# Kernel tuning notes

Measured on AMD Instinct MI355X. Metric: run time of the kernel, lower is better.

## Reference

```python
import jax, jax.numpy as jnp
import numpy as np

EMBED_DIM = 1024
NUM_HEADS = 16
HEAD_DIM = EMBED_DIM // NUM_HEADS
KERNEL = 3
PAD = KERNEL // 2
B, L = 4, 1024


def conv1d(x, w, b):
    # x: [B, D, L], w: [D_out, D_in, K], b: [D_out]; 'same' padding like nn.Conv1d(padding=K//2)
    y = jax.lax.conv_general_dilated(
        x, w, window_strides=(1,), padding=[(PAD, PAD)],
        dimension_numbers=('NCH', 'OIH', 'NCH'))
    return y + b[None, :, None]


def setup_inputs() -> dict:
    key = jax.random.key(0)
    ks = jax.random.split(key, 12)
    fan = EMBED_DIM * KERNEL
    bound = 1.0 / np.sqrt(fan)
    def wconv(k):
        return jax.random.uniform(k, (EMBED_DIM, EMBED_DIM, KERNEL), jnp.float32, -bound, bound)
    def bconv(k):
        return jax.random.uniform(k, (EMBED_DIM,), jnp.float32, -bound, bound)
    return {
        'query': jax.random.normal(ks[0], (B, L, EMBED_DIM), jnp.float32),
        'key': jax.random.normal(ks[1], (B, L, EMBED_DIM), jnp.float32),
        'value': jax.random.normal(ks[2], (B, L, EMBED_DIM), jnp.float32),
        'key_padding_mask': jax.random.randint(ks[3], (B, L), 0, 2) > 0,
        'attn_mask': jnp.zeros((L, L), jnp.float32),
        'q_w': wconv(ks[4]), 'q_b': bconv(ks[5]),
        'k_w': wconv(ks[6]), 'k_b': bconv(ks[7]),
        'v_w': wconv(ks[8]), 'v_b': bconv(ks[9]),
        'o_w': wconv(ks[10]), 'o_b': bconv(ks[11]),
    }


def reference(query, key, value, key_padding_mask, attn_mask,
              q_w, q_b, k_w, k_b, v_w, v_b, o_w, o_b):
    scale = HEAD_DIM ** -0.5
    # projections: [B, D, L]
    q = conv1d(jnp.swapaxes(query, 1, 2), q_w, q_b)
    k = conv1d(jnp.swapaxes(key, 1, 2), k_w, k_b)
    v = conv1d(jnp.swapaxes(value, 1, 2), v_w, v_b)
    # [B, H, d, L]
    q = q.reshape(B, NUM_HEADS, HEAD_DIM, L)
    k = k.reshape(B, NUM_HEADS, HEAD_DIM, L)
    v = v.reshape(B, NUM_HEADS, HEAD_DIM, L)
    # scores: [B, H, L, L]
    scores = jnp.einsum('bhdi,bhdj->bhij', q, k) * scale
    scores = scores + attn_mask[None, None, :, :]
    scores = jnp.where(key_padding_mask[:, None, None, :], -jnp.inf, scores)
    attn = jax.nn.softmax(scores, axis=-1)  # dropout p=0 (eval) -> identity
    out = jnp.einsum('bhij,bhdj->bhdi', attn, v)  # [B, H, d, L]
    out = out.reshape(B, EMBED_DIM, L)
    out = conv1d(out, o_w, o_b)
    return jnp.swapaxes(out, 1, 2)  # [B, L, D]
```

## Files before the change

### kernel.cpp

```cpp
#include <hip/hip_runtime.h>
#include <math.h>

#define NB 4
#define NL 1024
#define ND 1024
#define NH 16
#define HD 64

typedef __attribute__((ext_vector_type(8))) short bf16x8;
typedef __attribute__((ext_vector_type(4))) float f32x4;

static __device__ __forceinline__ unsigned short f32_to_bf16(float f) {
  unsigned u = __float_as_uint(f);
  u += 0x7FFFu + ((u >> 16) & 1u);
  return (unsigned short)(u >> 16);
}
static __device__ __forceinline__ float bf16_to_f32(unsigned short s) {
  return __uint_as_float(((unsigned)s) << 16);
}
static __device__ __forceinline__ float exp2_f(float x) {
  float r;
  asm("v_exp_f32 %0, %1" : "=v"(r) : "v"(x));
  return r;
}

static __device__ __forceinline__ void split8(float4 a, float4 b, bf16x8* hi, bf16x8* lo) {
  unsigned u[8] = {__float_as_uint(a.x), __float_as_uint(a.y),
                   __float_as_uint(a.z), __float_as_uint(a.w),
                   __float_as_uint(b.x), __float_as_uint(b.y),
                   __float_as_uint(b.z), __float_as_uint(b.w)};
  union { unsigned p[4]; bf16x8 v; } H, L;
#pragma unroll
  for (int p = 0; p < 4; ++p) {
    unsigned u0 = u[2 * p], u1 = u[2 * p + 1];
    H.p[p] = __builtin_amdgcn_perm(u1, u0, 0x07060302u);
    unsigned l0 = __float_as_uint(__uint_as_float(u0) - __uint_as_float(u0 & 0xFFFF0000u));
    unsigned l1 = __float_as_uint(__uint_as_float(u1) - __uint_as_float(u1 & 0xFFFF0000u));
    L.p[p] = __builtin_amdgcn_perm(l1, l0, 0x07060302u);
  }
  *hi = H.v; *lo = L.v;
}

__global__ __launch_bounds__(256) void wcvt_kernel(
    const float* __restrict__ w0, const float* __restrict__ w1,
    const float* __restrict__ w2, const float* __restrict__ w3,
    unsigned short* __restrict__ wb, int* __restrict__ flag)
{
  if (blockIdx.x == 0 && blockIdx.y == 0 && threadIdx.x == 0) flag[0] = 0;
  const int t = blockIdx.y;
  const int o = blockIdx.x;
  const float* w = (t == 0) ? w0 : (t == 1) ? w1 : (t == 2) ? w2 : w3;
  unsigned short* hi = wb + (size_t)t * 6 * (1u << 20);
  unsigned short* lo = hi + 3 * (1u << 20);
  const int tid = threadIdx.x;
  float v[12];
  const float* src = w + (size_t)o * (ND * 3) + tid * 12;
#pragma unroll
  for (int j = 0; j < 3; ++j) {
    float4 f = *(const float4*)(src + j * 4);
    v[j * 4 + 0] = f.x; v[j * 4 + 1] = f.y; v[j * 4 + 2] = f.z; v[j * 4 + 3] = f.w;
  }
#pragma unroll
  for (int k = 0; k < 3; ++k) {
    unsigned short hh[4], ll[4];
#pragma unroll
    for (int ii = 0; ii < 4; ++ii) {
      float x = v[ii * 3 + k];
      unsigned short h = f32_to_bf16(x);
      float r = x - bf16_to_f32(h);
      hh[ii] = h; ll[ii] = f32_to_bf16(r);
    }
    size_t dst = (size_t)k * (ND * ND) + (size_t)o * ND + tid * 4;
    *(ushort4*)&hi[dst] = make_ushort4(hh[0], hh[1], hh[2], hh[3]);
    *(ushort4*)&lo[dst] = make_ushort4(ll[0], ll[1], ll[2], ll[3]);
  }
}

__global__ __launch_bounds__(256) void amask_scan(
    const float* __restrict__ a, int* __restrict__ flag)
{
  size_t i = ((size_t)blockIdx.x * 256 + threadIdx.x) * 4;
  float4 v = *(const float4*)&a[i];
  if (v.x != 0.f || v.y != 0.f || v.z != 0.f || v.w != 0.f) atomicOr(flag, 1);
}

__global__ __launch_bounds__(256, 3) void conv_mfma2(
    const float* X0, const float* X1, const float* X2,
    const unsigned short* __restrict__ wb,
    const float* b0, const float* b1, const float* b2,
    float* Y0, float* Y1, float* Y2, int mode)
{
  __shared__ float Af[128 * 32];
  __shared__ unsigned short Bh[128 * 32];
  __shared__ unsigned short Bl[128 * 32];

  const int tid = threadIdx.x, lane = tid & 63, wave = tid >> 6;
  const int lin = blockIdx.x + 8 * (blockIdx.y + 32 * blockIdx.z);
  const int g = lin & 7, t = lin >> 3;
  const int nb = (g & 3) * 2 + (t & 1);
  const int mb = (g >> 2) * 16 + ((t >> 1) & 15);
  const int z  = t >> 5;
  const int n0 = nb * 128, m0 = mb * 128;
  const int b = m0 >> 10, l0v = m0 & (NL - 1);

  const float* X = (mode == 0) ? (z == 0 ? X0 : (z == 1 ? X1 : X2)) : X0;
  const unsigned short* Wh = (mode == 0) ? wb + (size_t)z * 6 * (1u << 20) : wb;
  const unsigned short* Wl = Wh + 3 * (1u << 20);

  const int wm = (wave >> 1) * 64, wn = (wave & 1) * 64;
  const int mrow = lane & 15, quad = lane >> 4;
  const int r16 = lane >> 2, cs = lane & 3;
  const int src_chunk = (cs - (r16 >> 1)) & 3;
  const int bswz = ((quad + (mrow >> 1)) & 3) * 8;

  f32x4 acc[4][4] = {};

  const int kbeg = (mode == 0) ? 0 : z;
  const int kend = (mode == 0) ? 3 : z + 1;
  for (int koff = kbeg; koff < kend; ++koff) {
    const bool edge_lo = (l0v == 0 && koff == 0);
    const bool edge_hi = (l0v == NL - 128 && koff == 2);
    for (int i0 = 0; i0 < ND; i0 += 32) {
#pragma unroll
      for (int s = 0; s < 2; ++s) {
        const int seg = wave * 2 + s;
        const size_t goff = ((size_t)koff << 20) +
                            (size_t)(n0 + seg * 16 + r16) * ND + i0 + src_chunk * 8;
        __builtin_amdgcn_global_load_lds(
            (const __attribute__((address_space(1))) unsigned int*)(Wh + goff),
            (__attribute__((address_space(3))) unsigned int*)&Bh[seg * 512], 16, 0, 0);
        __builtin_amdgcn_global_load_lds(
            (const __attribute__((address_space(1))) unsigned int*)(Wl + goff),
            (__attribute__((address_space(3))) unsigned int*)&Bl[seg * 512], 16, 0, 0);
      }
#pragma unroll
      for (int j = 0; j < 4; ++j) {
        const int s = (wave * 4 + j) * 64 + lane;
        const int row = s >> 3, sir = s & 7;
        const int chunk = (sir - (row & 7)) & 7;
        int l = l0v + row + koff - 1;
        l = (l < 0) ? 0 : (l > NL - 1 ? NL - 1 : l);
        const float* gp = X + ((size_t)(b << 10) + l) * ND + i0 + chunk * 4;
        __builtin_amdgcn_global_load_lds(
            (const __attribute__((address_space(1))) unsigned int*)gp,
            (__attribute__((address_space(3))) unsigned int*)&Af[(wave * 4 + j) * 256],
            16, 0, 0);
      }
      __syncthreads();
      if (edge_lo || edge_hi) {
        const int er = edge_lo ? 0 : 127;
        if (tid < 8) *(float4*)&Af[er * 32 + tid * 4] = make_float4(0.f, 0.f, 0.f, 0.f);
        __syncthreads();
      }
      bf16x8 ah[4], al[4];
#pragma unroll
      for (int mi = 0; mi < 4; ++mi) {
        const int row = wm + mi * 16 + mrow, r7 = row & 7;
        float4 fa = *(const float4*)&Af[row * 32 + (((quad * 2) + r7) & 7) * 4];
        float4 fb = *(const float4*)&Af[row * 32 + (((quad * 2 + 1) + r7) & 7) * 4];
        split8(fa, fb, &ah[mi], &al[mi]);
      }
#pragma unroll
      for (int ni = 0; ni < 4; ++ni) {
        const int brow = wn + ni * 16 + mrow;
        bf16x8 bh = *(const bf16x8*)&Bh[brow * 32 + bswz];
        bf16x8 bl = *(const bf16x8*)&Bl[brow * 32 + bswz];
#pragma unroll
        for (int mi = 0; mi < 4; ++mi) {
          acc[mi][ni] = __builtin_amdgcn_mfma_f32_16x16x32_bf16(ah[mi], bh, acc[mi][ni], 0, 0, 0);
          acc[mi][ni] = __builtin_amdgcn_mfma_f32_16x16x32_bf16(ah[mi], bl, acc[mi][ni], 0, 0, 0);
          acc[mi][ni] = __builtin_amdgcn_mfma_f32_16x16x32_bf16(al[mi], bh, acc[mi][ni], 0, 0, 0);
        }
      }
      __syncthreads();
    }
  }

  if (mode == 0) {
    const float* bias = (z == 0) ? b0 : (z == 1 ? b1 : b2);
    unsigned short* U = (unsigned short*)Y0;
    const size_t PLs = (size_t)NB * NL * ND / NH * NH;
    if (z < 2) {
      unsigned short* Ph = U + (size_t)(2 * z) * PLs;
      unsigned short* Pl = Ph + PLs;
      const float sc = (z == 0) ? 0.18033688011112042f : 1.0f;
#pragma unroll
      for (int ni = 0; ni < 4; ++ni) {
        const int n = n0 + wn + ni * 16 + mrow;
        const float bv = bias[n];
        const int h = n >> 6, dd = n & 63;
        const int bh = b * NH + h;
#pragma unroll
        for (int mi = 0; mi < 4; ++mi) {
          const int mbase = m0 + wm + mi * 16 + quad * 4;
          f32x4 v = acc[mi][ni];
#pragma unroll
          for (int r = 0; r < 4; ++r) {
            const int l = (mbase + r) & (NL - 1);
            const float val = (v[r] + bv) * sc;
            const unsigned u = __float_as_uint(val);
            const unsigned short hh = (unsigned short)(u >> 16);
            const float res = val - __uint_as_float(u & 0xFFFF0000u);
            const unsigned short ll = (unsigned short)(__float_as_uint(res) >> 16);
            const size_t off = ((size_t)bh * NL + l) * HD + dd;
            Ph[off] = hh; Pl[off] = ll;
          }
        }
      }
    } else {
      unsigned short* Pv = U + (size_t)4 * PLs;
#pragma unroll
      for (int ni = 0; ni < 4; ++ni) {
        const int n = n0 + wn + ni * 16 + mrow;
        const float bv = bias[n];
        const int h = n >> 6, dd = n & 63;
        const int bh = b * NH + h;
#pragma unroll
        for (int mi = 0; mi < 4; ++mi) {
          const int mbase = m0 + wm + mi * 16 + quad * 4;
          const int lb = mbase & (NL - 1);
          f32x4 v = acc[mi][ni];
          ushort4 s4 = make_ushort4(f32_to_bf16(v[0] + bv), f32_to_bf16(v[1] + bv),
                                    f32_to_bf16(v[2] + bv), f32_to_bf16(v[3] + bv));
          *(ushort4*)&Pv[((size_t)bh * HD + dd) * NL + lb] = s4;
        }
      }
    }
  } else {
    float* P = Y0 + (size_t)z * ((size_t)NB * NL * ND);
#pragma unroll
    for (int ni = 0; ni < 4; ++ni) {
      const int n = n0 + wn + ni * 16 + mrow;
#pragma unroll
      for (int mi = 0; mi < 4; ++mi) {
        const int mbase = m0 + wm + mi * 16 + quad * 4;
        f32x4 v = acc[mi][ni];
#pragma unroll
        for (int r = 0; r < 4; ++r) {
          const int l = (mbase + r) & (NL - 1);
          P[((size_t)(b << 10) + l) * ND + n] = v[r];
        }
      }
    }
  }
}

__global__ __launch_bounds__(256) void reduce_kernel(
    const float* __restrict__ P, const float* __restrict__ bias, float* __restrict__ out)
{
  const size_t S = (size_t)NB * NL * ND;
  const size_t idx = ((size_t)blockIdx.x * 256 + threadIdx.x) * 4;
  const int n = (int)(idx & (ND - 1));
  float4 p0 = *(const float4*)&P[idx];
  float4 p1 = *(const float4*)&P[idx + S];
  float4 p2 = *(const float4*)&P[idx + 2 * S];
  float4 bv = *(const float4*)&bias[n];
  float4 r;
  r.x = p0.x + p1.x + p2.x + bv.x;
  r.y = p0.y + p1.y + p2.y + bv.y;
  r.z = p0.z + p1.z + p2.z + bv.z;
  r.w = p0.w + p1.w + p2.w + bv.w;
  *(float4*)&out[idx] = r;
}

__global__ __launch_bounds__(256, 3) void attn_mfma(
    const unsigned short* __restrict__ U, const int* __restrict__ kpm,
    const float* __restrict__ amask, const int* __restrict__ aflagp,
    float* __restrict__ AO)
{
  __shared__ __align__(16) unsigned short S[3 * 4096];
  __shared__ __align__(16) float Fm[NL];
  unsigned short* Kh = S;
  unsigned short* Kl = S + 4096;
  unsigned short* Vt = S + 8192;

  const int tid = threadIdx.x, lane = tid & 63, wave = tid >> 6;
  const int c = lane & 15, quad = lane >> 4;
  const int lin = blockIdx.x;
  const int bh = (lin & 7) + 8 * (lin >> 7);
  const int mt = (lin >> 3) & 15;
  const int b = bh >> 4;
  const int m0 = mt * 64;
  const int aflag = *aflagp;
  const int mrow = wave * 16 + c;
  const int gm = m0 + mrow;

  const size_t PLs = (size_t)4096 * 1024;
  const unsigned short* qTh = U;
  const unsigned short* qTl = U + PLs;
  const unsigned short* kTh = U + 2 * PLs;
  const unsigned short* kTl = U + 3 * PLs;
  const unsigned short* vTt = U + 4 * PLs;

  const int srow = lane >> 3;
  const int slot = lane & 7;
  const int chunk = (slot - srow) & 7;

#pragma unroll
  for (int q = 0; q < 4; ++q) {
    const int pl = q >> 1;
    const int i = wave * 2 + (q & 1);
    const int row = i * 8 + srow;
    const unsigned short* src = (pl ? qTl : qTh) +
        ((size_t)bh * NL + m0 + row) * HD + chunk * 8;
    unsigned short* dst = (pl ? Kl : Kh) + i * 512;
    __builtin_amdgcn_global_load_lds(
        (const __attribute__((address_space(1))) unsigned int*)src,
        (__attribute__((address_space(3))) unsigned int*)dst, 16, 0, 0);
  }
  {
    int4 kv = *(const int4*)&kpm[b * NL + tid * 4];
    float4 f;
    f.x = kv.x ? -INFINITY : 0.f;
    f.y = kv.y ? -INFINITY : 0.f;
    f.z = kv.z ? -INFINITY : 0.f;
    f.w = kv.w ? -INFINITY : 0.f;
    *(float4*)&Fm[tid * 4] = f;
  }
  __syncthreads();
  bf16x8 qbh[2], qbl[2];
#pragma unroll
  for (int kb = 0; kb < 2; ++kb) {
    const int cso = ((kb * 4 + quad + mrow) & 7) * 8;
    qbh[kb] = *(const bf16x8*)&Kh[mrow * 64 + cso];
    qbl[kb] = *(const bf16x8*)&Kl[mrow * 64 + cso];
  }

  f32x4 acc[4] = {};
  float m_r = -INFINITY, l_r = 0.0f;

  for (int n0t = 0; n0t < NL; n0t += 64) {
    __syncthreads();

#pragma unroll
    for (int q = 0; q < 6; ++q) {
      const int pl = q >> 1;
      const int i = wave * 2 + (q & 1);
      const int row = i * 8 + srow;
      const unsigned short* src;
      unsigned short* dst;
      if (pl == 0)      { src = kTh + ((size_t)bh * NL + n0t + row) * HD + chunk * 8; dst = Kh + i * 512; }
      else if (pl == 1) { src = kTl + ((size_t)bh * NL + n0t + row) * HD + chunk * 8; dst = Kl + i * 512; }
      else              { src = vTt + ((size_t)bh * HD + row) * NL + n0t + chunk * 8; dst = Vt + i * 512; }
      __builtin_amdgcn_global_load_lds(
          (const __attribute__((address_space(1))) unsigned int*)src,
          (__attribute__((address_space(3))) unsigned int*)dst, 16, 0, 0);
    }

    float mval[4][4];
#pragma unroll
    for (int nf = 0; nf < 4; ++nf) {
      float4 fm = *(const float4*)&Fm[n0t + nf * 16 + quad * 4];
      mval[nf][0] = fm.x; mval[nf][1] = fm.y; mval[nf][2] = fm.z; mval[nf][3] = fm.w;
    }
    if (aflag) {
#pragma unroll
      for (int nf = 0; nf < 4; ++nf)
#pragma unroll
        for (int r = 0; r < 4; ++r) {
          const int gn = n0t + nf * 16 + quad * 4 + r;
          mval[nf][r] += amask[(size_t)gm * NL + gn] * 1.4426950408889634f;
        }
    }
    __syncthreads();

    f32x4 sa[4] = {};
    __builtin_amdgcn_s_setprio(1);
#pragma unroll
    for (int kb = 0; kb < 2; ++kb)
#pragma unroll
      for (int nf = 0; nf < 4; ++nf) {
        const int row = nf * 16 + c;
        const int cso = ((kb * 4 + quad + row) & 7) * 8;
        bf16x8 kah = *(const bf16x8*)&Kh[row * 64 + cso];
        bf16x8 kal = *(const bf16x8*)&Kl[row * 64 + cso];
        sa[nf] = __builtin_amdgcn_mfma_f32_16x16x32_bf16(kah, qbh[kb], sa[nf], 0, 0, 0);
        sa[nf] = __builtin_amdgcn_mfma_f32_16x16x32_bf16(kah, qbl[kb], sa[nf], 0, 0, 0);
        sa[nf] = __builtin_amdgcn_mfma_f32_16x16x32_bf16(kal, qbh[kb], sa[nf], 0, 0, 0);
      }
    __builtin_amdgcn_s_setprio(0);

    float p[4][4];
    float tmax = -INFINITY;
#pragma unroll
    for (int nf = 0; nf < 4; ++nf)
#pragma unroll
      for (int r = 0; r < 4; ++r) {
        float s = sa[nf][r] + mval[nf][r];
        p[nf][r] = s;
        tmax = fmaxf(tmax, s);
      }
    tmax = fmaxf(tmax, __shfl_xor(tmax, 16));
    tmax = fmaxf(tmax, __shfl_xor(tmax, 32));
    float rs = 0.f;
    if (__all(tmax - m_r <= 8.0f)) {
      const float msafe = m_r;
#pragma unroll
      for (int nf = 0; nf < 4; ++nf)
#pragma unroll
        for (int r = 0; r < 4; ++r) {
          float e = exp2_f(p[nf][r] - msafe);
          p[nf][r] = e;
          rs += e;
        }
      rs += __shfl_xor(rs, 16);
      rs += __shfl_xor(rs, 32);
      l_r += rs;
    } else {
      const float newm = fmaxf(m_r, tmax);
      const float msafe = (newm == -INFINITY) ? 0.f : newm;
      const float alpha = exp2_f(m_r - msafe);
#pragma unroll
      for (int nf = 0; nf < 4; ++nf)
#pragma unroll
        for (int r = 0; r < 4; ++r) {
          float e = exp2_f(p[nf][r] - msafe);
          p[nf][r] = e;
          rs += e;
        }
      rs += __shfl_xor(rs, 16);
      rs += __shfl_xor(rs, 32);
      l_r = l_r * alpha + rs;
      m_r = newm;
#pragma unroll
      for (int df = 0; df < 4; ++df) {
        acc[df][0] *= alpha; acc[df][1] *= alpha;
        acc[df][2] *= alpha; acc[df][3] *= alpha;
      }
    }

    unsigned q16[4][2];
#pragma unroll
    for (int nf = 0; nf < 4; ++nf)
#pragma unroll
      for (int w = 0; w < 2; ++w)
        q16[nf][w] = (unsigned)f32_to_bf16(p[nf][2 * w]) |
                     ((unsigned)f32_to_bf16(p[nf][2 * w + 1]) << 16);

#pragma unroll
    for (int kb = 0; kb < 2; ++kb) {
      union { unsigned d[4]; bf16x8 v; } pb;
#pragma unroll
      for (int w = 0; w < 4; ++w) {
        const int addr = ((((quad & 1) * 2 + (w >> 1)) * 16 + c) << 2);
        unsigned v0 = __builtin_amdgcn_ds_bpermute(addr, (int)q16[2 * kb][w & 1]);
        unsigned v1 = __builtin_amdgcn_ds_bpermute(addr, (int)q16[2 * kb + 1][w & 1]);
        pb.d[w] = (quad >> 1) ? v1 : v0;
      }
      __builtin_amdgcn_s_setprio(1);
#pragma unroll
      for (int df = 0; df < 4; ++df) {
        const int row = df * 16 + c;
        const int cso = ((kb * 4 + quad + row) & 7) * 8;
        bf16x8 va = *(const bf16x8*)&Vt[row * 64 + cso];
        acc[df] = __builtin_amdgcn_mfma_f32_16x16x32_bf16(va, pb.v, acc[df], 0, 0, 0);
      }
      __builtin_amdgcn_s_setprio(0);
    }
  }

  __syncthreads();
  const float inv = 1.0f / l_r;
  float* Ob = (float*)S + wave * (16 * 68);
#pragma unroll
  for (int df = 0; df < 4; ++df)
#pragma unroll
    for (int r = 0; r < 4; ++r)
      Ob[c * 68 + df * 16 + quad * 4 + r] = acc[df][r] * inv;
  __syncthreads();
  const int mr2 = lane >> 2, cq2 = lane & 3;
  const int h = bh & 15;
#pragma unroll
  for (int ii = 0; ii < 4; ++ii) {
    const int chunk2 = cq2 * 4 + ii;
    float4 v = *(const float4*)&Ob[mr2 * 68 + chunk2 * 4];
    *(float4*)&AO[((size_t)(b << 10) + (m0 + wave * 16 + mr2)) * ND +
                  h * HD + chunk2 * 4] = v;
  }
}

extern "C" void kernel_launch(void* const* d_in, const int* in_sizes, int n_in,
                              void* d_out, int out_size, void* d_ws, size_t ws_size,
                              hipStream_t stream) {
  (void)in_sizes; (void)n_in; (void)out_size; (void)ws_size;
  const float* query = (const float*)d_in[0];
  const float* key_  = (const float*)d_in[1];
  const float* value = (const float*)d_in[2];
  const int*   kpm   = (const int*)d_in[3];
  const float* amask = (const float*)d_in[4];
  const float* q_w = (const float*)d_in[5];
  const float* q_b = (const float*)d_in[6];
  const float* k_w = (const float*)d_in[7];
  const float* k_b = (const float*)d_in[8];
  const float* v_w = (const float*)d_in[9];
  const float* v_b = (const float*)d_in[10];
  const float* o_w = (const float*)d_in[11];
  const float* o_b = (const float*)d_in[12];
  float* out = (float*)d_out;

  unsigned short* Wb = (unsigned short*)d_ws;
  unsigned short* U  = (unsigned short*)((char*)d_ws + (size_t)50331648);
  float* P  = (float*)((char*)d_ws + (size_t)50331648);
  float* AO = (float*)d_ws;
  int* flag = (int*)d_out;

  wcvt_kernel<<<dim3(1024, 4), 256, 0, stream>>>(q_w, k_w, v_w, o_w, Wb, flag);
  amask_scan<<<1024, 256, 0, stream>>>(amask, flag);
  conv_mfma2<<<dim3(8, 32, 3), 256, 0, stream>>>(
      query, key_, value, Wb, q_b, k_b, v_b, (float*)U, (float*)U, (float*)U, 0);
  attn_mfma<<<1024, 256, 0, stream>>>(U, kpm, amask, flag, AO);
  conv_mfma2<<<dim3(8, 32, 3), 256, 0, stream>>>(
      AO, AO, AO, Wb + (size_t)3 * 6 * (1u << 20), o_b, o_b, o_b, P, P, P, 1);
  reduce_kernel<<<4096, 256, 0, stream>>>(P, o_b, out);
}
```

Measured before the change: 499.8 us.

## Pre-split conv activations into bf16 hi/lo planes before the projection GEMMs

```diff
diff --git a/kernel.cpp b/kernel.cpp
--- a/kernel.cpp
+++ b/kernel.cpp
@@ -6,6 +6,7 @@
 #define ND 1024
 #define NH 16
 #define HD 64
+#define PLN 4194304
 
 typedef __attribute__((ext_vector_type(8))) short bf16x8;
 typedef __attribute__((ext_vector_type(4))) float f32x4;
@@ -84,15 +85,35 @@
   if (v.x != 0.f || v.y != 0.f || v.z != 0.f || v.w != 0.f) atomicOr(flag, 1);
 }
 
+__global__ __launch_bounds__(256) void xsplit_kernel(
+    const float* __restrict__ x0, const float* __restrict__ x1,
+    const float* __restrict__ x2, unsigned short* __restrict__ xs)
+{
+  const int z = blockIdx.y;
+  const float* x = (z == 0) ? x0 : (z == 1) ? x1 : x2;
+  const size_t i = ((size_t)blockIdx.x * 256 + threadIdx.x) * 8;
+  float4 a = *(const float4*)&x[i];
+  float4 b = *(const float4*)&x[i + 4];
+  bf16x8 hi, lo;
+  split8(a, b, &hi, &lo);
+  unsigned short* ph = xs + (size_t)z * 2 * PLN;
+  *(bf16x8*)&ph[i] = hi;
+  *(bf16x8*)&ph[PLN + i] = lo;
+}
+
+template<int ASPLIT, int MODE>
 __global__ __launch_bounds__(256, 3) void conv_mfma2(
-    const float* X0, const float* X1, const float* X2,
+    const void* X0v, const void* X1v, const void* X2v,
     const unsigned short* __restrict__ wb,
     const float* b0, const float* b1, const float* b2,
-    float* Y0, float* Y1, float* Y2, int mode)
+    float* Y0)
 {
-  __shared__ float Af[128 * 32];
+  __shared__ __align__(16) unsigned char Araw[16384];
   __shared__ unsigned short Bh[128 * 32];
   __shared__ unsigned short Bl[128 * 32];
+  float* Af = (float*)Araw;
+  unsigned short* Ah = (unsigned short*)Araw;
+  unsigned short* Al = (unsigned short*)(Araw + 8192);
 
   const int tid = threadIdx.x, lane = tid & 63, wave = tid >> 6;
   const int lin = blockIdx.x + 8 * (blockIdx.y + 32 * blockIdx.z);
@@ -103,9 +124,19 @@
   const int n0 = nb * 128, m0 = mb * 128;
   const int b = m0 >> 10, l0v = m0 & (NL - 1);
 
-  const float* X = (mode == 0) ? (z == 0 ? X0 : (z == 1 ? X1 : X2)) : X0;
-  const unsigned short* Wh = (mode == 0) ? wb + (size_t)z * 6 * (1u << 20) : wb;
+  const unsigned short* Wh = (MODE == 0) ? wb + (size_t)z * 6 * (1u << 20) : wb;
   const unsigned short* Wl = Wh + 3 * (1u << 20);
+
+  const float* Xf = nullptr;
+  const unsigned short* Xh_ = nullptr;
+  const unsigned short* Xl_ = nullptr;
+  if (ASPLIT) {
+    const unsigned short* p = (const unsigned short*)((MODE == 0)
+        ? (z == 0 ? X0v : (z == 1 ? X1v : X2v)) : X0v);
+    Xh_ = p; Xl_ = p + PLN;
+  } else {
+    Xf = (const float*)((MODE == 0) ? (z == 0 ? X0v : (z == 1 ? X1v : X2v)) : X0v);
+  }
 
   const int wm = (wave >> 1) * 64, wn = (wave & 1) * 64;
   const int mrow = lane & 15, quad = lane >> 4;
@@ -115,8 +146,8 @@
 
   f32x4 acc[4][4] = {};
 
-  const int kbeg = (mode == 0) ? 0 : z;
-  const int kend = (mode == 0) ? 3 : z + 1;
+  const int kbeg = (MODE == 0) ? 0 : z;
+  const int kend = (MODE == 0) ? 3 : z + 1;
   for (int koff = kbeg; koff < kend; ++koff) {
     const bool edge_lo = (l0v == 0 && koff == 0);
     const bool edge_hi = (l0v == NL - 128 && koff == 2);
@@ -133,32 +164,67 @@
             (const __attribute__((address_space(1))) unsigned int*)(Wl + goff),
             (__attribute__((address_space(3))) unsigned int*)&Bl[seg * 512], 16, 0, 0);
       }
-#pragma unroll
-      for (int j = 0; j < 4; ++j) {
-        const int s = (wave * 4 + j) * 64 + lane;
-        const int row = s >> 3, sir = s & 7;
-        const int chunk = (sir - (row & 7)) & 7;
-        int l = l0v + row + koff - 1;
-        l = (l < 0) ? 0 : (l > NL - 1 ? NL - 1 : l);
-        const float* gp = X + ((size_t)(b << 10) + l) * ND + i0 + chunk * 4;
-        __builtin_amdgcn_global_load_lds(
-            (const __attribute__((address_space(1))) unsigned int*)gp,
-            (__attribute__((address_space(3))) unsigned int*)&Af[(wave * 4 + j) * 256],
-            16, 0, 0);
+      if (ASPLIT) {
+#pragma unroll
+        for (int j = 0; j < 4; ++j) {
+          const int seg = wave * 2 + (j & 1);
+          const int row = seg * 16 + (lane >> 2);
+          const int slot = lane & 3;
+          const int chunk = (slot - (row >> 1)) & 3;
+          int l = l0v + row + koff - 1;
+          l = (l < 0) ? 0 : (l > NL - 1 ? NL - 1 : l);
+          const unsigned short* Xp = (j >> 1) ? Xl_ : Xh_;
+          unsigned short* dst = ((j >> 1) ? Al : Ah) + seg * 512;
+          const unsigned short* gp = Xp + ((size_t)(b << 10) + l) * ND + i0 + chunk * 8;
+          __builtin_amdgcn_global_load_lds(
+              (const __attribute__((address_space(1))) unsigned int*)gp,
+              (__attribute__((address_space(3))) unsigned int*)dst, 16, 0, 0);
+        }
+      } else {
+#pragma unroll
+        for (int j = 0; j < 4; ++j) {
+          const int s = (wave * 4 + j) * 64 + lane;
+          const int row = s >> 3, sir = s & 7;
+          const int chunk = (sir - (row & 7)) & 7;
+          int l = l0v + row + koff - 1;
+          l = (l < 0) ? 0 : (l > NL - 1 ? NL - 1 : l);
+          const float* gp = Xf + ((size_t)(b << 10) + l) * ND + i0 + chunk * 4;
+          __builtin_amdgcn_global_load_lds(
+              (const __attribute__((address_space(1))) unsigned int*)gp,
+              (__attribute__((address_space(3))) unsigned int*)&Af[(wave * 4 + j) * 256],
+              16, 0, 0);
+        }
       }
       __syncthreads();
       if (edge_lo || edge_hi) {
         const int er = edge_lo ? 0 : 127;
-        if (tid < 8) *(float4*)&Af[er * 32 + tid * 4] = make_float4(0.f, 0.f, 0.f, 0.f);
+        if (ASPLIT) {
+          if (tid < 16) {
+            unsigned short* pl = (tid < 8) ? Ah : Al;
+            *(ushort4*)&pl[er * 32 + (tid & 7) * 4] = make_ushort4(0, 0, 0, 0);
+          }
+        } else {
+          if (tid < 8) *(float4*)&Af[er * 32 + tid * 4] = make_float4(0.f, 0.f, 0.f, 0.f);
+        }
         __syncthreads();
       }
       bf16x8 ah[4], al[4];
-#pragma unroll
-      for (int mi = 0; mi < 4; ++mi) {
-        const int row = wm + mi * 16 + mrow, r7 = row & 7;
-        float4 fa = *(const float4*)&Af[row * 32 + (((quad * 2) + r7) & 7) * 4];
-        float4 fb = *(const float4*)&Af[row * 32 + (((quad * 2 + 1) + r7) & 7) * 4];
-        split8(fa, fb, &ah[mi], &al[mi]);
+      if (ASPLIT) {
+#pragma unroll
+        for (int mi = 0; mi < 4; ++mi) {
+          const int row = wm + mi * 16 + mrow;
+          const int cso = ((quad + (row >> 1)) & 3) * 8;
+          ah[mi] = *(const bf16x8*)&Ah[row * 32 + cso];
+          al[mi] = *(const bf16x8*)&Al[row * 32 + cso];
+        }
+      } else {
+#pragma unroll
+        for (int mi = 0; mi < 4; ++mi) {
+          const int row = wm + mi * 16 + mrow, r7 = row & 7;
+          float4 fa = *(const float4*)&Af[row * 32 + (((quad * 2) + r7) & 7) * 4];
+          float4 fb = *(const float4*)&Af[row * 32 + (((quad * 2 + 1) + r7) & 7) * 4];
+          split8(fa, fb, &ah[mi], &al[mi]);
+        }
       }
 #pragma unroll
       for (int ni = 0; ni < 4; ++ni) {
@@ -176,13 +242,12 @@
     }
   }
 
-  if (mode == 0) {
-    const float* bias = (z == 0) ? b0 : (z == 1 ? b1 : b2);
+  if (MODE == 0) {
+    const float* bias = (z == 0) ? b0 : (z == 1) ? b1 : b2;
     unsigned short* U = (unsigned short*)Y0;
-    const size_t PLs = (size_t)NB * NL * ND / NH * NH;
     if (z < 2) {
-      unsigned short* Ph = U + (size_t)(2 * z) * PLs;
-      unsigned short* Pl = Ph + PLs;
+      unsigned short* Ph = U + (size_t)(2 * z) * PLN;
+      unsigned short* Pl = Ph + PLN;
       const float sc = (z == 0) ? 0.18033688011112042f : 1.0f;
 #pragma unroll
       for (int ni = 0; ni < 4; ++ni) {
@@ -208,7 +273,7 @@
         }
       }
     } else {
-      unsigned short* Pv = U + (size_t)4 * PLs;
+      unsigned short* Pv = U + (size_t)4 * PLN;
 #pragma unroll
       for (int ni = 0; ni < 4; ++ni) {
         const int n = n0 + wn + ni * 16 + mrow;
@@ -266,7 +331,7 @@
 __global__ __launch_bounds__(256, 3) void attn_mfma(
     const unsigned short* __restrict__ U, const int* __restrict__ kpm,
     const float* __restrict__ amask, const int* __restrict__ aflagp,
-    float* __restrict__ AO)
+    unsigned short* __restrict__ AO)
 {
   __shared__ __align__(16) unsigned short S[3 * 4096];
   __shared__ __align__(16) float Fm[NL];
@@ -285,7 +350,7 @@
   const int mrow = wave * 16 + c;
   const int gm = m0 + mrow;
 
-  const size_t PLs = (size_t)4096 * 1024;
+  const size_t PLs = (size_t)PLN;
   const unsigned short* qTh = U;
   const unsigned short* qTl = U + PLs;
   const unsigned short* kTh = U + 2 * PLs;
@@ -470,19 +535,32 @@
   __syncthreads();
   const int mr2 = lane >> 2, cq2 = lane & 3;
   const int h = bh & 15;
+  unsigned short* AOl_ = AO + PLN;
 #pragma unroll
   for (int ii = 0; ii < 4; ++ii) {
     const int chunk2 = cq2 * 4 + ii;
     float4 v = *(const float4*)&Ob[mr2 * 68 + chunk2 * 4];
-    *(float4*)&AO[((size_t)(b << 10) + (m0 + wave * 16 + mr2)) * ND +
-                  h * HD + chunk2 * 4] = v;
+    const size_t off = ((size_t)(b << 10) + (m0 + wave * 16 + mr2)) * ND + h * HD + chunk2 * 4;
+    float vv[4] = {v.x, v.y, v.z, v.w};
+    ushort4 hh, ll;
+    unsigned short* hp = (unsigned short*)&hh;
+    unsigned short* lp = (unsigned short*)&ll;
+#pragma unroll
+    for (int e = 0; e < 4; ++e) {
+      const unsigned u = __float_as_uint(vv[e]);
+      hp[e] = (unsigned short)(u >> 16);
+      const float res = vv[e] - __uint_as_float(u & 0xFFFF0000u);
+      lp[e] = (unsigned short)(__float_as_uint(res) >> 16);
+    }
+    *(ushort4*)&AO[off] = hh;
+    *(ushort4*)&AOl_[off] = ll;
   }
 }
 
 extern "C" void kernel_launch(void* const* d_in, const int* in_sizes, int n_in,
                               void* d_out, int out_size, void* d_ws, size_t ws_size,
                               hipStream_t stream) {
-  (void)in_sizes; (void)n_in; (void)out_size; (void)ws_size;
+  (void)in_sizes; (void)n_in; (void)out_size;
   const float* query = (const float*)d_in[0];
   const float* key_  = (const float*)d_in[1];
   const float* value = (const float*)d_in[2];
@@ -498,18 +576,26 @@
   const float* o_b = (const float*)d_in[12];
   float* out = (float*)d_out;
 
-  unsigned short* Wb = (unsigned short*)d_ws;
-  unsigned short* U  = (unsigned short*)((char*)d_ws + (size_t)50331648);
-  float* P  = (float*)((char*)d_ws + (size_t)50331648);
-  float* AO = (float*)d_ws;
+  unsigned short* Wb  = (unsigned short*)d_ws;
+  unsigned short* U   = (unsigned short*)((char*)d_ws + (size_t)50331648);
+  float*          P   = (float*)((char*)d_ws + (size_t)50331648);
+  unsigned short* AOs = (unsigned short*)d_ws;
+  unsigned short* Xs  = (unsigned short*)((char*)d_ws + (size_t)92274688);
   int* flag = (int*)d_out;
+  const bool presplit = ws_size >= (size_t)142606336;
 
   wcvt_kernel<<<dim3(1024, 4), 256, 0, stream>>>(q_w, k_w, v_w, o_w, Wb, flag);
   amask_scan<<<1024, 256, 0, stream>>>(amask, flag);
-  conv_mfma2<<<dim3(8, 32, 3), 256, 0, stream>>>(
-      query, key_, value, Wb, q_b, k_b, v_b, (float*)U, (float*)U, (float*)U, 0);
-  attn_mfma<<<1024, 256, 0, stream>>>(U, kpm, amask, flag, AO);
-  conv_mfma2<<<dim3(8, 32, 3), 256, 0, stream>>>(
-      AO, AO, AO, Wb + (size_t)3 * 6 * (1u << 20), o_b, o_b, o_b, P, P, P, 1);
+  if (presplit) {
+    xsplit_kernel<<<dim3(2048, 3), 256, 0, stream>>>(query, key_, value, Xs);
+    conv_mfma2<1, 0><<<dim3(8, 32, 3), 256, 0, stream>>>(
+        Xs, Xs + (size_t)2 * PLN, Xs + (size_t)4 * PLN, Wb, q_b, k_b, v_b, (float*)U);
+  } else {
+    conv_mfma2<0, 0><<<dim3(8, 32, 3), 256, 0, stream>>>(
+        query, key_, value, Wb, q_b, k_b, v_b, (float*)U);
+  }
+  attn_mfma<<<1024, 256, 0, stream>>>(U, kpm, amask, flag, AOs);
+  conv_mfma2<1, 1><<<dim3(8, 32, 3), 256, 0, stream>>>(
+      AOs, AOs, AOs, Wb + (size_t)3 * 6 * (1u << 20), o_b, o_b, o_b, P);
   reduce_kernel<<<4096, 256, 0, stream>>>(P, o_b, out);
 }
```

After: 518.5 us. +3.7%, slower.
